# Kernel optimization log

Measured on AMD Instinct MI355X. Metric: run time of the kernel, lower is better.

The kernel has to match this reference:

```python
import jax, jax.numpy as jnp
import numpy as np

N_NODES = 100000
N_EDGES = 1600000
IN_C, HID, OUT_C = 128, 128, 64
N_LAYERS = 4


def setup_inputs() -> dict:
    key = jax.random.key(0)
    ks = jax.random.split(key, 12)
    s_in = 1.0 / np.sqrt(IN_C)
    s_h = 1.0 / np.sqrt(HID)
    x = jax.random.normal(ks[0], (N_NODES, IN_C), dtype=jnp.float32)
    edge_index = jax.random.randint(ks[1], (2, N_EDGES), 0, N_NODES, dtype=jnp.int64)
    return {
        "x": x,
        "edge_index": edge_index,
        "W_in": jax.random.uniform(ks[2], (IN_C, HID), jnp.float32, -s_in, s_in),
        "b_in": jax.random.uniform(ks[3], (HID,), jnp.float32, -s_in, s_in),
        "W_conv": jax.random.uniform(ks[4], (N_LAYERS, HID, HID), jnp.float32, -s_h, s_h),
        "b_conv": jax.random.uniform(ks[5], (N_LAYERS, HID), jnp.float32, -s_h, s_h),
        "alpha": 0.1 * jax.random.normal(ks[6], (N_LAYERS,), jnp.float32),
        "beta": 1.0 + 0.1 * jax.random.normal(ks[7], (N_LAYERS,), jnp.float32),
        "W_out": jax.random.uniform(ks[8], (HID, OUT_C), jnp.float32, -s_h, s_h),
        "b_out": jax.random.uniform(ks[9], (OUT_C,), jnp.float32, -s_h, s_h),
    }


def _gcn_norm(edge_index, n_nodes):
    # add self-loops, symmetric deg^-1/2 normalization (PyG gcn_norm, edge_weight=1)
    loop = jnp.arange(n_nodes, dtype=edge_index.dtype)
    src = jnp.concatenate([edge_index[0], loop])
    dst = jnp.concatenate([edge_index[1], loop])
    deg = jax.ops.segment_sum(jnp.ones_like(dst, dtype=jnp.float32), dst, n_nodes)
    dinv = jnp.where(deg > 0, jax.lax.rsqrt(deg), 0.0)
    norm = dinv[src] * dinv[dst]  # [E + N]
    return src, dst, norm


def _gcn_conv(h, W, b, src, dst, norm, n_nodes):
    h = h @ W                                 # [N, HID]
    msg = h[src] * norm[:, None]              # gather + scale, [E+N, HID]
    agg = jax.ops.segment_sum(msg, dst, n_nodes)  # scatter-add back to nodes
    return agg + b


def reference(x, edge_index, W_in, b_in, W_conv, b_conv, alpha, beta, W_out, b_out):
    n = x.shape[0]
    src, dst, norm = _gcn_norm(edge_index, n)
    h = x @ W_in + b_in
    inp = h
    for i in range(N_LAYERS):
        h = _gcn_conv(inp, W_conv[i], b_conv[i], src, dst, norm, n)
        h = jnp.tanh(h)                        # activation='Tanh'; dropout p=0
        h = beta[i] * inp + alpha[i] * h       # rezero residual
        inp = h
    logits = h @ W_out + b_out
    return jax.nn.log_softmax(logits, axis=1)
```

## Files before the change

kernel.cpp:

```cpp
#include <hip/hip_runtime.h>
#include <cstdint>
#include <cstddef>


constexpr int K = 128;

typedef __bf16 bf16x8 __attribute__((ext_vector_type(8)));
typedef float f32x4 __attribute__((ext_vector_type(4)));
typedef float f32x2 __attribute__((ext_vector_type(2)));

__device__ inline uint16_t f2bf(float f) {
    union { float f; uint32_t u; } c; c.f = f;
    uint32_t r = (c.u + 0x7fffu + ((c.u >> 16) & 1u)) >> 16;
    return (uint16_t)r;
}
__device__ inline float blo(uint32_t u) { union { uint32_t i; float f; } c; c.i = u << 16; return c.f; }
__device__ inline float bhi(uint32_t u) { union { uint32_t i; float f; } c; c.i = u & 0xffff0000u; return c.f; }

__device__ inline float fast_tanh(float x) {
    union { float f; uint32_t u; } cx; cx.f = x;
    uint32_t sgn = cx.u & 0x80000000u;
    cx.u &= 0x7fffffffu;
    float t = __expf(2.0f * cx.f);
    float r = fmaf(-2.0f, __builtin_amdgcn_rcpf(t + 1.0f), 1.0f);
    union { float f; uint32_t u; } cr; cr.f = r;
    cr.u |= sgn;
    return cr.f;
}


__global__ __launch_bounds__(256) void s1_hist(const int* __restrict__ dst,
                                               int* __restrict__ ghist, int E) {
    __shared__ int hist[1024];
    for (int i = threadIdx.x; i < 1024; i += 256) hist[i] = 0;
    __syncthreads();
    int stride = gridDim.x * 256;
    for (int e = blockIdx.x * 256 + threadIdx.x; e < E; e += stride)
        atomicAdd(&hist[dst[e] >> 7], 1);
    __syncthreads();
    for (int i = threadIdx.x; i < 1024; i += 256) {
        int c = hist[i];
        if (c) atomicAdd(&ghist[i], c);
    }
}

__global__ void s2_scan(const int* __restrict__ ghist, int* __restrict__ gbase,
                        int* __restrict__ gcur, int* __restrict__ off, int N, int E) {
    __shared__ int buf[1024];
    int t = threadIdx.x;
    int v = ghist[t];
    buf[t] = v;
    __syncthreads();
    for (int o = 1; o < 1024; o <<= 1) {
        int add = (t >= o) ? buf[t - o] : 0;
        __syncthreads();
        buf[t] += add;
        __syncthreads();
    }
    int ex = buf[t] - v;
    gbase[t] = ex;
    gcur[t] = ex;
    if (t == 1023) gbase[1024] = buf[1023];
    if (t == 0) off[N] = E;
}

__global__ __launch_bounds__(256) void s3_scatter(
    const int* __restrict__ src, const int* __restrict__ dst,
    int* __restrict__ gcur, int* __restrict__ ebuf, int E)
{
    __shared__ int hist[1024], base[1024], cursor[1024];
    const int t = threadIdx.x;
    const int tile = blockIdx.x * 4096;
    for (int i = t; i < 1024; i += 256) { hist[i] = 0; cursor[i] = 0; }
    __syncthreads();
    int sv[16], dv[16];
#pragma unroll
    for (int k = 0; k < 16; ++k) {
        int e = tile + k * 256 + t;
        bool ok = e < E;
        sv[k] = ok ? src[e] : -1;
        dv[k] = ok ? dst[e] : 0;
        if (ok) atomicAdd(&hist[dv[k] >> 7], 1);
    }
    __syncthreads();
    for (int i = t; i < 1024; i += 256) {
        int c = hist[i];
        base[i] = c ? atomicAdd(&gcur[i], c) : 0;
    }
    __syncthreads();
#pragma unroll
    for (int k = 0; k < 16; ++k) {
        if (sv[k] >= 0) {
            int b = dv[k] >> 7;
            int r = atomicAdd(&cursor[b], 1);
            ebuf[base[b] + r] = (sv[k] << 7) | (dv[k] & 127);
        }
    }
}

__global__ __launch_bounds__(256) void s4_finalize(
    const int* __restrict__ gbase, const int* __restrict__ ebuf,
    int* __restrict__ csr, int* __restrict__ off, float* __restrict__ dinv,
    int N, int E)
{
    __shared__ int hist[128], excl[128], cursor[128];
    const int b = blockIdx.x;
    const int t = threadIdx.x;
    const int lo = gbase[b], hi = gbase[b + 1];
    if (t < 128) hist[t] = 0;
    __syncthreads();
    for (int i = lo + t; i < hi; i += 256) atomicAdd(&hist[ebuf[i] & 127], 1);
    __syncthreads();
    if (t < 128) excl[t] = hist[t];
    __syncthreads();
    for (int o = 1; o < 128; o <<= 1) {
        int v = (t < 128 && t >= o) ? excl[t - o] : 0;
        __syncthreads();
        if (t < 128) excl[t] += v;
        __syncthreads();
    }
    if (t < 128) {
        int node = b * 128 + t;
        int ex = excl[t] - hist[t];
        cursor[t] = ex;
        if (node < N) {
            off[node] = lo + ex;
            dinv[node] = rsqrtf((float)hist[t] + 1.0f);
        }
    }
    __syncthreads();
    for (int i = lo + t; i < hi; i += 256) {
        int v = ebuf[i];
        int r = atomicAdd(&cursor[v & 127], 1);
        csr[lo + r] = v & ~127;
    }
}


__global__ void wconv_all(const float* __restrict__ Win, const float* __restrict__ Wc,
                          const float* __restrict__ Wo, uint16_t* __restrict__ Tin,
                          uint16_t* __restrict__ Tc, uint16_t* __restrict__ To) {
    int idx = blockIdx.x * 256 + threadIdx.x;
    if (idx < 16384) {
        int c = idx >> 7, k = idx & 127;
        Tin[idx] = f2bf(Win[k * 128 + c]);
    } else if (idx < 81920) {
        int t = idx - 16384;
        int l = t >> 14, li = t & 16383;
        int c = li >> 7, k = li & 127;
        Tc[t] = f2bf(Wc[l * 16384 + k * 128 + c]);
    } else if (idx < 90112) {
        int t = idx - 81920;
        int c = t >> 7, k = t & 127;
        To[t] = f2bf(Wo[k * 64 + c]);
    }
}


template <int NOUT, bool A_FP32, int OMODE>
__global__ __launch_bounds__(256) void mfma_gemm(
    const void* __restrict__ Aptr, const uint16_t* __restrict__ Wt,
    const float* __restrict__ bias, float* __restrict__ outF,
    uint16_t* __restrict__ outB, uint8_t* __restrict__ outQ,
    const float* __restrict__ rowscale, int M)
{
    constexpr int NT = NOUT / 16;
    const int tid = threadIdx.x;
    const int w = tid >> 6;
    const int l = tid & 63;
    const int lg = l >> 4;
    const int lr = l & 15;
    const int rbase = blockIdx.x * 128 + w * 32;
    const int r0c = min(rbase + lr, M - 1);
    const int r1c = min(rbase + 16 + lr, M - 1);

    f32x4 acc[2][NT] = {};

    for (int k0 = 0; k0 < K; k0 += 32) {
        const int ka = k0 + lg * 8;
        bf16x8 a0, a1;
        if constexpr (A_FP32) {
            const float* A = (const float*)Aptr;
            const float* p0 = A + (size_t)r0c * K + ka;
            const float* p1 = A + (size_t)r1c * K + ka;
            float4 u0 = *(const float4*)p0, v0 = *(const float4*)(p0 + 4);
            float4 u1 = *(const float4*)p1, v1 = *(const float4*)(p1 + 4);
            a0[0] = (__bf16)u0.x; a0[1] = (__bf16)u0.y; a0[2] = (__bf16)u0.z; a0[3] = (__bf16)u0.w;
            a0[4] = (__bf16)v0.x; a0[5] = (__bf16)v0.y; a0[6] = (__bf16)v0.z; a0[7] = (__bf16)v0.w;
            a1[0] = (__bf16)u1.x; a1[1] = (__bf16)u1.y; a1[2] = (__bf16)u1.z; a1[3] = (__bf16)u1.w;
            a1[4] = (__bf16)v1.x; a1[5] = (__bf16)v1.y; a1[6] = (__bf16)v1.z; a1[7] = (__bf16)v1.w;
        } else {
            const uint16_t* A = (const uint16_t*)Aptr;
            a0 = *reinterpret_cast<const bf16x8*>(A + (size_t)r0c * K + ka);
            a1 = *reinterpret_cast<const bf16x8*>(A + (size_t)r1c * K + ka);
        }
#pragma unroll
        for (int ct = 0; ct < NT; ++ct) {
            bf16x8 b = *reinterpret_cast<const bf16x8*>(Wt + (size_t)(ct * 16 + lr) * K + ka);
            acc[0][ct] = __builtin_amdgcn_mfma_f32_16x16x32_bf16(a0, b, acc[0][ct], 0, 0, 0);
            acc[1][ct] = __builtin_amdgcn_mfma_f32_16x16x32_bf16(a1, b, acc[1][ct], 0, 0, 0);
        }
    }

    float bv[NT];
    if constexpr (OMODE == 0 || OMODE == 1) {
#pragma unroll
        for (int ct = 0; ct < NT; ++ct) bv[ct] = bias[ct * 16 + lr];
    }

    if constexpr (OMODE == 1) {
#pragma unroll
        for (int t = 0; t < 2; ++t) {
#pragma unroll
            for (int i = 0; i < 4; ++i) {
                float v[NT];
                float m = -3.0e38f;
#pragma unroll
                for (int ct = 0; ct < NT; ++ct) {
                    v[ct] = acc[t][ct][i] + bv[ct];
                    m = fmaxf(m, v[ct]);
                }
#pragma unroll
                for (int o = 8; o >= 1; o >>= 1) m = fmaxf(m, __shfl_xor(m, o));
                float s = 0.f;
#pragma unroll
                for (int ct = 0; ct < NT; ++ct) s += __expf(v[ct] - m);
#pragma unroll
                for (int o = 8; o >= 1; o >>= 1) s += __shfl_xor(s, o);
                float lse = m + __logf(s);
                int rr = rbase + t * 16 + lg * 4 + i;
                if (rr < M) {
#pragma unroll
                    for (int ct = 0; ct < NT; ++ct)
                        outF[(size_t)rr * NOUT + ct * 16 + lr] = v[ct] - lse;
                }
            }
        }
    } else {
#pragma unroll
        for (int t = 0; t < 2; ++t) {
#pragma unroll
            for (int i = 0; i < 4; ++i) {
                int rr = rbase + t * 16 + lg * 4 + i;
                if (rr < M) {
                    float sc = 1.0f;
                    if constexpr (OMODE == 2) sc = rowscale[rr];
#pragma unroll
                    for (int ct = 0; ct < NT; ++ct) {
                        float v = acc[t][ct][i];
                        size_t o = (size_t)rr * NOUT + ct * 16 + lr;
                        if constexpr (OMODE == 0) {
                            outB[o] = f2bf(v + bv[ct]);
                        } else {
                            v *= sc;
                            int pk = __builtin_amdgcn_cvt_pk_fp8_f32(v, v, 0, false);
                            outQ[o] = (uint8_t)(pk & 0xff);
                        }
                    }
                }
            }
        }
    }
}


__global__ __launch_bounds__(256) void agg_kernel(
    const uint8_t* __restrict__ B, uint16_t* __restrict__ A,
    const float* __restrict__ dinv, const int* __restrict__ off,
    const int* __restrict__ csr, const float* __restrict__ bconv,
    const float* __restrict__ alpha, const float* __restrict__ beta,
    int n, int E)
{
    int gid = blockIdx.x * 256 + threadIdx.x;
    int d = gid >> 6;
    int lane = threadIdx.x & 63;
    if (d >= n) return;

    const int half = lane >> 5;
    const int c0 = (lane & 31) * 4;
    f32x2 acc01 = {0.f, 0.f}, acc23 = {0.f, 0.f};
    const int s0 = off[d], s1 = off[d + 1];

    for (int j0 = s0; j0 < s1; j0 += 64) {
        int idx = j0 + lane;
        int sv = csr[min(idx, E - 1)];
        const int cnt = min(64, s1 - j0);
        const int cf = cnt & ~7;
        int it = 0;
        for (; it < cf; it += 8) {
            uint32_t u[4];
#pragma unroll
            for (int q = 0; q < 4; ++q) {
                int o = __shfl(sv, it + 2 * q + half);
                u[q] = *(const uint32_t*)(B + o + c0);
            }
#pragma unroll
            for (int q = 0; q < 4; ++q) {
                acc01 += __builtin_amdgcn_cvt_pk_f32_fp8((int)u[q], false);
                acc23 += __builtin_amdgcn_cvt_pk_f32_fp8((int)u[q], true);
            }
        }
        if (it < cnt) {
            uint32_t u[4];
#pragma unroll
            for (int q = 0; q < 4; ++q) {
                int e = it + 2 * q + half;
                int o = __shfl(sv, e);
                u[q] = (e < cnt) ? *(const uint32_t*)(B + o + c0) : 0u;
            }
#pragma unroll
            for (int q = 0; q < 4; ++q) {
                acc01 += __builtin_amdgcn_cvt_pk_f32_fp8((int)u[q], false);
                acc23 += __builtin_amdgcn_cvt_pk_f32_fp8((int)u[q], true);
            }
        }
    }
    float a0 = acc01[0], a1 = acc01[1], a2 = acc23[0], a3 = acc23[1];
    a0 += __shfl_xor(a0, 32); a1 += __shfl_xor(a1, 32);
    a2 += __shfl_xor(a2, 32); a3 += __shfl_xor(a3, 32);
    {
        uint32_t u = *(const uint32_t*)(B + ((size_t)d << 7) + c0);
        f32x2 lo = __builtin_amdgcn_cvt_pk_f32_fp8((int)u, false);
        f32x2 hi = __builtin_amdgcn_cvt_pk_f32_fp8((int)u, true);
        a0 += lo[0]; a1 += lo[1]; a2 += hi[0]; a3 += hi[1];
    }

    float dd = dinv[d];
    float al = alpha[0], be = beta[0];
    float4 bb = *(const float4*)(bconv + c0);
    uint2 ip = *(const uint2*)(A + (size_t)d * K + c0);
    float o0 = be * blo(ip.x) + al * fast_tanh(fmaf(dd, a0, bb.x));
    float o1 = be * bhi(ip.x) + al * fast_tanh(fmaf(dd, a1, bb.y));
    float o2 = be * blo(ip.y) + al * fast_tanh(fmaf(dd, a2, bb.z));
    float o3 = be * bhi(ip.y) + al * fast_tanh(fmaf(dd, a3, bb.w));
    if (half == 0) {
        uint2 pk;
        asm("v_cvt_pk_bf16_f32 %0, %1, %2" : "=v"(pk.x) : "v"(o0), "v"(o1));
        asm("v_cvt_pk_bf16_f32 %0, %1, %2" : "=v"(pk.y) : "v"(o2), "v"(o3));
        *(uint2*)(A + (size_t)d * K + c0) = pk;
    }
}


extern "C" void kernel_launch(void* const* d_in, const int* in_sizes, int n_in,
                              void* d_out, int out_size, void* d_ws, size_t ws_size,
                              hipStream_t stream)
{
    const float* x      = (const float*)d_in[0];
    const int*   ei     = (const int*)d_in[1];
    const float* W_in   = (const float*)d_in[2];
    const float* b_in   = (const float*)d_in[3];
    const float* W_conv = (const float*)d_in[4];
    const float* b_conv = (const float*)d_in[5];
    const float* alpha  = (const float*)d_in[6];
    const float* beta   = (const float*)d_in[7];
    const float* W_out  = (const float*)d_in[8];
    const float* b_out  = (const float*)d_in[9];
    float* out = (float*)d_out;

    const int N = in_sizes[0] / K;
    const int E = in_sizes[1] / 2;
    const int L = in_sizes[6];

    const int* src = ei;
    const int* dst = ei + E;

    char* p = (char*)d_ws;
    uint16_t* Abf = (uint16_t*)p;      p += (size_t)N * K * sizeof(uint16_t);
    uint8_t* Bq8 = (uint8_t*)p;        p += (size_t)N * K * sizeof(uint8_t);
    uint16_t* Wt_in = (uint16_t*)p;    p += (size_t)K * K * sizeof(uint16_t);
    uint16_t* Wt_conv = (uint16_t*)p;  p += (size_t)4 * K * K * sizeof(uint16_t);
    uint16_t* Wt_out = (uint16_t*)p;   p += (size_t)64 * K * sizeof(uint16_t);
    float* dinv = (float*)p;           p += (size_t)N * sizeof(float);
    int* off = (int*)p;                p += (size_t)(N + 1) * sizeof(int);
    int* csr = (int*)p;                p += (size_t)E * sizeof(int);
    int* ghist = (int*)p;              p += 1024 * sizeof(int);
    int* gbase = (int*)p;              p += 1025 * sizeof(int);
    int* gcur = (int*)p;               p += 1024 * sizeof(int);
    int* ebuf = (int*)p;               p += (size_t)E * sizeof(int);

    hipMemsetAsync(ghist, 0, 1024 * sizeof(int), stream);
    s1_hist<<<256, 256, 0, stream>>>(dst, ghist, E);
    s2_scan<<<1, 1024, 0, stream>>>(ghist, gbase, gcur, off, N, E);
    s3_scatter<<<(E + 4095) / 4096, 256, 0, stream>>>(src, dst, gcur, ebuf, E);
    s4_finalize<<<(N + 127) / 128, 256, 0, stream>>>(gbase, ebuf, csr, off, dinv, N, E);

    wconv_all<<<(90112 + 255) / 256, 256, 0, stream>>>(
        W_in, W_conv, W_out, Wt_in, Wt_conv, Wt_out);

    const int gblocks = (N + 127) / 128;
    mfma_gemm<128, true, 0><<<gblocks, 256, 0, stream>>>(
        x, Wt_in, b_in, nullptr, Abf, nullptr, nullptr, N);
    for (int l = 0; l < L; ++l) {
        mfma_gemm<128, false, 2><<<gblocks, 256, 0, stream>>>(
            Abf, Wt_conv + (size_t)l * K * K, nullptr, nullptr, nullptr, Bq8, dinv, N);
        agg_kernel<<<(N * 64 + 255) / 256, 256, 0, stream>>>(
            Bq8, Abf, dinv, off, csr, b_conv + (size_t)l * K,
            alpha + l, beta + l, N, E);
    }
    mfma_gemm<64, false, 1><<<gblocks, 256, 0, stream>>>(
        Abf, Wt_out, b_out, out, nullptr, nullptr, nullptr, N);
}
```

Before: 494.4 us.

## Fuse independent preprocessing kernels into shared launches to overlap CSR build and GEMM

Merges the destination histogram with the weight bf16 transpose into one launch, and the input projection GEMM with the edge-scatter stage into another, by dispatching on block index. This removes two kernel launches and lets independent work fill the GPU at the same time. The scatter stage also doubles per-block tile size (32 edges per thread), which raises register pressure in the fused kernel and may lower occupancy for the GEMM blocks that share it.

Result: no change. 488.9 us (-1.1%).

```diff
diff --git a/kernel.cpp b/kernel.cpp
--- a/kernel.cpp
+++ b/kernel.cpp
@@ -29,13 +29,13 @@
 }
 
 
-__global__ __launch_bounds__(256) void s1_hist(const int* __restrict__ dst,
-                                               int* __restrict__ ghist, int E) {
+__device__ __forceinline__ void s1_body(int bid, const int* __restrict__ dst,
+                                        int* __restrict__ ghist, int E) {
     __shared__ int hist[1024];
     for (int i = threadIdx.x; i < 1024; i += 256) hist[i] = 0;
     __syncthreads();
-    int stride = gridDim.x * 256;
-    for (int e = blockIdx.x * 256 + threadIdx.x; e < E; e += stride)
+    int stride = 256 * 256;
+    for (int e = bid * 256 + threadIdx.x; e < E; e += stride)
         atomicAdd(&hist[dst[e] >> 7], 1);
     __syncthreads();
     for (int i = threadIdx.x; i < 1024; i += 256) {
@@ -44,103 +44,13 @@
     }
 }
 
-__global__ void s2_scan(const int* __restrict__ ghist, int* __restrict__ gbase,
-                        int* __restrict__ gcur, int* __restrict__ off, int N, int E) {
-    __shared__ int buf[1024];
-    int t = threadIdx.x;
-    int v = ghist[t];
-    buf[t] = v;
-    __syncthreads();
-    for (int o = 1; o < 1024; o <<= 1) {
-        int add = (t >= o) ? buf[t - o] : 0;
-        __syncthreads();
-        buf[t] += add;
-        __syncthreads();
-    }
-    int ex = buf[t] - v;
-    gbase[t] = ex;
-    gcur[t] = ex;
-    if (t == 1023) gbase[1024] = buf[1023];
-    if (t == 0) off[N] = E;
-}
-
-__global__ __launch_bounds__(256) void s3_scatter(
-    const int* __restrict__ src, const int* __restrict__ dst,
-    int* __restrict__ gcur, int* __restrict__ ebuf, int E)
-{
-    __shared__ int hist[1024], base[1024], cursor[1024];
-    const int t = threadIdx.x;
-    const int tile = blockIdx.x * 4096;
-    for (int i = t; i < 1024; i += 256) { hist[i] = 0; cursor[i] = 0; }
-    __syncthreads();
-    int sv[16], dv[16];
-#pragma unroll
-    for (int k = 0; k < 16; ++k) {
-        int e = tile + k * 256 + t;
-        bool ok = e < E;
-        sv[k] = ok ? src[e] : -1;
-        dv[k] = ok ? dst[e] : 0;
-        if (ok) atomicAdd(&hist[dv[k] >> 7], 1);
-    }
-    __syncthreads();
-    for (int i = t; i < 1024; i += 256) {
-        int c = hist[i];
-        base[i] = c ? atomicAdd(&gcur[i], c) : 0;
-    }
-    __syncthreads();
-#pragma unroll
-    for (int k = 0; k < 16; ++k) {
-        if (sv[k] >= 0) {
-            int b = dv[k] >> 7;
-            int r = atomicAdd(&cursor[b], 1);
-            ebuf[base[b] + r] = (sv[k] << 7) | (dv[k] & 127);
-        }
-    }
-}
-
-__global__ __launch_bounds__(256) void s4_finalize(
-    const int* __restrict__ gbase, const int* __restrict__ ebuf,
-    int* __restrict__ csr, int* __restrict__ off, float* __restrict__ dinv,
-    int N, int E)
-{
-    __shared__ int hist[128], excl[128], cursor[128];
-    const int b = blockIdx.x;
-    const int t = threadIdx.x;
-    const int lo = gbase[b], hi = gbase[b + 1];
-    if (t < 128) hist[t] = 0;
-    __syncthreads();
-    for (int i = lo + t; i < hi; i += 256) atomicAdd(&hist[ebuf[i] & 127], 1);
-    __syncthreads();
-    if (t < 128) excl[t] = hist[t];
-    __syncthreads();
-    for (int o = 1; o < 128; o <<= 1) {
-        int v = (t < 128 && t >= o) ? excl[t - o] : 0;
-        __syncthreads();
-        if (t < 128) excl[t] += v;
-        __syncthreads();
-    }
-    if (t < 128) {
-        int node = b * 128 + t;
-        int ex = excl[t] - hist[t];
-        cursor[t] = ex;
-        if (node < N) {
-            off[node] = lo + ex;
-            dinv[node] = rsqrtf((float)hist[t] + 1.0f);
-        }
-    }
-    __syncthreads();
-    for (int i = lo + t; i < hi; i += 256) {
-        int v = ebuf[i];
-        int r = atomicAdd(&cursor[v & 127], 1);
-        csr[lo + r] = v & ~127;
-    }
-}
-
-
-__global__ void wconv_all(const float* __restrict__ Win, const float* __restrict__ Wc,
-                          const float* __restrict__ Wo, uint16_t* __restrict__ Tin,
-                          uint16_t* __restrict__ Tc, uint16_t* __restrict__ To) {
-    int idx = blockIdx.x * 256 + threadIdx.x;
+__device__ __forceinline__ void wconv_body(int bid, const float* __restrict__ Win,
+                                           const float* __restrict__ Wc,
+                                           const float* __restrict__ Wo,
+                                           uint16_t* __restrict__ Tin,
+                                           uint16_t* __restrict__ Tc,
+                                           uint16_t* __restrict__ To) {
+    int idx = bid * 256 + threadIdx.x;
     if (idx < 16384) {
         int c = idx >> 7, k = idx & 127;
         Tin[idx] = f2bf(Win[k * 128 + c]);
@@ -156,10 +66,113 @@
     }
 }
 
+__global__ __launch_bounds__(256) void fused_s1_wconv(
+    const int* __restrict__ dst, int* __restrict__ ghist, int E,
+    const float* __restrict__ Win, const float* __restrict__ Wc,
+    const float* __restrict__ Wo, uint16_t* __restrict__ Tin,
+    uint16_t* __restrict__ Tc, uint16_t* __restrict__ To)
+{
+    int b = blockIdx.x;
+    if (b < 256) s1_body(b, dst, ghist, E);
+    else wconv_body(b - 256, Win, Wc, Wo, Tin, Tc, To);
+}
+
+__global__ void s2_scan(const int* __restrict__ ghist, int* __restrict__ gbase,
+                        int* __restrict__ gcur, int* __restrict__ off, int N, int E) {
+    __shared__ int buf[1024];
+    int t = threadIdx.x;
+    int v = ghist[t];
+    buf[t] = v;
+    __syncthreads();
+    for (int o = 1; o < 1024; o <<= 1) {
+        int add = (t >= o) ? buf[t - o] : 0;
+        __syncthreads();
+        buf[t] += add;
+        __syncthreads();
+    }
+    int ex = buf[t] - v;
+    gbase[t] = ex;
+    gcur[t] = ex;
+    if (t == 1023) gbase[1024] = buf[1023];
+    if (t == 0) off[N] = E;
+}
+
+__device__ __forceinline__ void s3_body(int bid, const int* __restrict__ src,
+                                        const int* __restrict__ dst,
+                                        int* __restrict__ gcur,
+                                        int* __restrict__ ebuf, int E) {
+    __shared__ int hist[1024], base[1024], cursor[1024];
+    const int t = threadIdx.x;
+    const int tile = bid * 8192;
+    for (int i = t; i < 1024; i += 256) { hist[i] = 0; cursor[i] = 0; }
+    __syncthreads();
+    int sv[32], dv[32];
+#pragma unroll
+    for (int k = 0; k < 32; ++k) {
+        int e = tile + k * 256 + t;
+        bool ok = e < E;
+        sv[k] = ok ? src[e] : -1;
+        dv[k] = ok ? dst[e] : 0;
+        if (ok) atomicAdd(&hist[dv[k] >> 7], 1);
+    }
+    __syncthreads();
+    for (int i = t; i < 1024; i += 256) {
+        int c = hist[i];
+        base[i] = c ? atomicAdd(&gcur[i], c) : 0;
+    }
+    __syncthreads();
+#pragma unroll
+    for (int k = 0; k < 32; ++k) {
+        if (sv[k] >= 0) {
+            int b = dv[k] >> 7;
+            int r = atomicAdd(&cursor[b], 1);
+            ebuf[base[b] + r] = (sv[k] << 7) | (dv[k] & 127);
+        }
+    }
+}
+
+__global__ __launch_bounds__(256) void s4_finalize(
+    const int* __restrict__ gbase, const int* __restrict__ ebuf,
+    int* __restrict__ csr, int* __restrict__ off, float* __restrict__ dinv,
+    int N, int E)
+{
+    __shared__ int hist[128], excl[128], cursor[128];
+    const int b = blockIdx.x;
+    const int t = threadIdx.x;
+    const int lo = gbase[b], hi = gbase[b + 1];
+    if (t < 128) hist[t] = 0;
+    __syncthreads();
+    for (int i = lo + t; i < hi; i += 256) atomicAdd(&hist[ebuf[i] & 127], 1);
+    __syncthreads();
+    if (t < 128) excl[t] = hist[t];
+    __syncthreads();
+    for (int o = 1; o < 128; o <<= 1) {
+        int v = (t < 128 && t >= o) ? excl[t - o] : 0;
+        __syncthreads();
+        if (t < 128) excl[t] += v;
+        __syncthreads();
+    }
+    if (t < 128) {
+        int node = b * 128 + t;
+        int ex = excl[t] - hist[t];
+        cursor[t] = ex;
+        if (node < N) {
+            off[node] = lo + ex;
+            dinv[node] = rsqrtf((float)hist[t] + 1.0f);
+        }
+    }
+    __syncthreads();
+    for (int i = lo + t; i < hi; i += 256) {
+        int v = ebuf[i];
+        int r = atomicAdd(&cursor[v & 127], 1);
+        csr[lo + r] = v & ~127;
+    }
+}
+
 
 template <int NOUT, bool A_FP32, int OMODE>
-__global__ __launch_bounds__(256) void mfma_gemm(
-    const void* __restrict__ Aptr, const uint16_t* __restrict__ Wt,
+__device__ __forceinline__ void gemm_body(
+    int bid, const void* __restrict__ Aptr, const uint16_t* __restrict__ Wt,
     const float* __restrict__ bias, float* __restrict__ outF,
     uint16_t* __restrict__ outB, uint8_t* __restrict__ outQ,
     const float* __restrict__ rowscale, int M)
@@ -170,7 +183,7 @@
     const int l = tid & 63;
     const int lg = l >> 4;
     const int lr = l & 15;
-    const int rbase = blockIdx.x * 128 + w * 32;
+    const int rbase = bid * 128 + w * 32;
     const int r0c = min(rbase + lr, M - 1);
     const int r1c = min(rbase + 16 + lr, M - 1);
 
@@ -263,6 +276,29 @@
     }
 }
 
+template <int NOUT, bool A_FP32, int OMODE>
+__global__ __launch_bounds__(256) void mfma_gemm(
+    const void* __restrict__ Aptr, const uint16_t* __restrict__ Wt,
+    const float* __restrict__ bias, float* __restrict__ outF,
+    uint16_t* __restrict__ outB, uint8_t* __restrict__ outQ,
+    const float* __restrict__ rowscale, int M)
+{
+    gemm_body<NOUT, A_FP32, OMODE>(blockIdx.x, Aptr, Wt, bias, outF, outB, outQ, rowscale, M);
+}
+
+__global__ __launch_bounds__(256) void fused_gin_s3(
+    const void* __restrict__ Aptr, const uint16_t* __restrict__ Wt,
+    const float* __restrict__ bias, uint16_t* __restrict__ outB, int M, int gblocks,
+    const int* __restrict__ src, const int* __restrict__ dst,
+    int* __restrict__ gcur, int* __restrict__ ebuf, int E)
+{
+    int b = blockIdx.x;
+    if (b < gblocks)
+        gemm_body<128, true, 0>(b, Aptr, Wt, bias, nullptr, outB, nullptr, nullptr, M);
+    else
+        s3_body(b - gblocks, src, dst, gcur, ebuf, E);
+}
+
 
 __global__ __launch_bounds__(256) void agg_kernel(
     const uint8_t* __restrict__ B, uint16_t* __restrict__ A,
@@ -379,18 +415,17 @@
     int* gcur = (int*)p;               p += 1024 * sizeof(int);
     int* ebuf = (int*)p;               p += (size_t)E * sizeof(int);
 
+    const int gblocks = (N + 127) / 128;
+    const int s3blocks = (E + 8191) / 8192;
+
     hipMemsetAsync(ghist, 0, 1024 * sizeof(int), stream);
-    s1_hist<<<256, 256, 0, stream>>>(dst, ghist, E);
+    fused_s1_wconv<<<256 + 352, 256, 0, stream>>>(
+        dst, ghist, E, W_in, W_conv, W_out, Wt_in, Wt_conv, Wt_out);
     s2_scan<<<1, 1024, 0, stream>>>(ghist, gbase, gcur, off, N, E);
-    s3_scatter<<<(E + 4095) / 4096, 256, 0, stream>>>(src, dst, gcur, ebuf, E);
-    s4_finalize<<<(N + 127) / 128, 256, 0, stream>>>(gbase, ebuf, csr, off, dinv, N, E);
-
-    wconv_all<<<(90112 + 255) / 256, 256, 0, stream>>>(
-        W_in, W_conv, W_out, Wt_in, Wt_conv, Wt_out);
-
-    const int gblocks = (N + 127) / 128;
-    mfma_gemm<128, true, 0><<<gblocks, 256, 0, stream>>>(
-        x, Wt_in, b_in, nullptr, Abf, nullptr, nullptr, N);
+    fused_gin_s3<<<gblocks + s3blocks, 256, 0, stream>>>(
+        x, Wt_in, b_in, Abf, N, gblocks, src, dst, gcur, ebuf, E);
+    s4_finalize<<<gblocks, 256, 0, stream>>>(gbase, ebuf, csr, off, dinv, N, E);
+
     for (int l = 0; l < L; ++l) {
         mfma_gemm<128, false, 2><<<gblocks, 256, 0, stream>>>(
             Abf, Wt_conv + (size_t)l * K * K, nullptr, nullptr, nullptr, Bq8, dinv, N);
```
